# Performance work log

Hardware: AMD Instinct MI355X
Metric: run time of the kernel (lower is better)

## Reference

```python
import jax, jax.numpy as jnp
import numpy as np

N = 100000    # nodes
E = 1600000   # edges (avg degree 16)
IN = 128      # input feature dim
D = 32        # per-head hidden dim
H = 4         # heads for hidden layers
C = 16        # num_classes (final per-head dim)
NEG = 0.2     # leaky_relu negative slope


def setup_inputs() -> dict:
    key = jax.random.key(0)
    ks = jax.random.split(key, 14)
    s = jnp.float32(0.05)
    f32 = jnp.float32
    inp = {
        "inputs": jax.random.normal(ks[0], (N, IN), f32),
        "src": jax.random.randint(ks[1], (E,), 0, N),
        "dst": jax.random.randint(ks[2], (E,), 0, N),
        # layer 0: IN -> (H, D), no residual
        "W0": jax.random.normal(ks[3], (IN, H * D), f32) * s,
        "al0": jax.random.normal(ks[4], (H, D), f32) * s,
        "ar0": jax.random.normal(ks[5], (H, D), f32) * s,
        # layer 1: H*D -> (H, D), identity residual (dims match)
        "W1": jax.random.normal(ks[6], (H * D, H * D), f32) * s,
        "al1": jax.random.normal(ks[7], (H, D), f32) * s,
        "ar1": jax.random.normal(ks[8], (H, D), f32) * s,
        # final layer: H*D -> (1, C), linear residual projection
        "W2": jax.random.normal(ks[9], (H * D, 1 * C), f32) * s,
        "al2": jax.random.normal(ks[10], (1, C), f32) * s,
        "ar2": jax.random.normal(ks[11], (1, C), f32) * s,
        "resW2": jax.random.normal(ks[12], (H * D, 1 * C), f32) * s,
    }
    return inp


def gat_conv(h, W, al, ar, src, dst, n_heads, out_dim, res=None, act=None):
    # h: (N, F_in) -> out: (N, n_heads, out_dim)
    feat = (h @ W).reshape(N, n_heads, out_dim)            # (N,H,D)
    el = jnp.sum(feat * al, axis=-1)                       # (N,H)
    er = jnp.sum(feat * ar, axis=-1)                       # (N,H)
    e = jax.nn.leaky_relu(el[src] + er[dst], NEG)          # (E,H)
    # softmax over incoming edges per destination node
    emax = jax.ops.segment_max(e, dst, num_segments=N)     # (N,H)
    ex = jnp.exp(e - emax[dst])                            # (E,H)
    den = jax.ops.segment_sum(ex, dst, num_segments=N)     # (N,H)
    alpha = ex / den[dst]                                  # (E,H)
    msg = feat[src] * alpha[:, :, None]                    # (E,H,D) -- dominant traffic
    out = jax.ops.segment_sum(msg, dst, num_segments=N)    # (N,H,D)
    if res is not None:
        out = out + res
    if act is not None:
        out = act(out)
    return out


def reference(inputs, src, dst, W0, al0, ar0, W1, al1, ar1, W2, al2, ar2, resW2):
    # hidden layer 0 (no residual), GATConv activation = elu, then flatten + relu
    h = gat_conv(inputs, W0, al0, ar0, src, dst, H, D, res=None, act=jax.nn.elu)
    h = jax.nn.relu(h.reshape(N, H * D))
    # hidden layer 1, identity residual (in == H*D)
    res1 = h.reshape(N, H, D)
    h = gat_conv(h, W1, al1, ar1, src, dst, H, D, res=res1, act=jax.nn.elu)
    h = jax.nn.relu(h.reshape(N, H * D))
    # output layer: 1 head, linear residual projection, no activation, mean over heads
    res2 = (h @ resW2).reshape(N, 1, C)
    out = gat_conv(h, W2, al2, ar2, src, dst, 1, C, res=res2, act=None)
    return out.mean(axis=1)                                # (N, C)
```

## Files before the change

### kernel.cpp

```cpp
#include <hip/hip_runtime.h>

#define N_NODES 100000
#define N_EDGES 1600000
#define IN_F    128
#define NEG_SLOPE 0.2f
#define NBUCK   512
#define BCAP    5120
#define PCHUNK  4096
#define PGRID   391
#define GEMMGRID 1563

typedef __attribute__((ext_vector_type(8))) short bf16x8;
typedef __attribute__((ext_vector_type(4))) float f32x4;

__device__ __forceinline__ float bf2f(unsigned short u) {
    return __uint_as_float(((unsigned int)u) << 16);
}

__device__ __forceinline__ unsigned short f2bf(float f) {
    unsigned int u = __float_as_uint(f);
    u += 0x7FFFu + ((u >> 16) & 1u);
    return (unsigned short)(u >> 16);
}

__device__ __forceinline__ unsigned int ld_u32(const char* base, unsigned int off) {
    return *(const unsigned int*)(base + off);
}

__global__ __launch_bounds__(256) void init_pack(int* __restrict__ bcursor,
                                                 const float* __restrict__ W0,
                                                 const float* __restrict__ W1,
                                                 const float* __restrict__ W2,
                                                 const float* __restrict__ rW2,
                                                 unsigned short* __restrict__ W0p,
                                                 unsigned short* __restrict__ W1p,
                                                 unsigned short* __restrict__ W2p) {
    const int t = threadIdx.x;
    if (blockIdx.x < 2) {
        int i = blockIdx.x * 256 + t;
        if (i < NBUCK) bcursor[i] = i * BCAP;
        return;
    }
    int gid = (blockIdx.x - 2) * 256 + t;
    const float* W;
    unsigned short* Wp;
    int idx, ncols;
    if (gid < 16384)      { W = W0; Wp = W0p; idx = gid;          ncols = 128; }
    else if (gid < 32768) { W = W1; Wp = W1p; idx = gid - 16384;  ncols = 128; }
    else                  { W = W2; Wp = W2p; idx = gid - 32768;  ncols = 32;  }
    int j  = idx & 7;
    int l  = (idx >> 3) & 63;
    int kt = (idx >> 9) & 3;
    int nt = idx >> 11;
    int k  = kt * 32 + (l >> 4) * 8 + j;
    int n  = nt * 16 + (l & 15);
    float v;
    if (ncols == 128) v = W[k * 128 + n];
    else              v = (n < 16) ? W[k * 16 + n] : rW2[k * 16 + (n - 16)];
    Wp[idx] = f2bf(v);
}

__global__ __launch_bounds__(256) void part_gemm0(const int* __restrict__ src,
                                                  const int* __restrict__ dst,
                                                  int* __restrict__ bcursor,
                                                  unsigned int* __restrict__ pe, int nE,
                                                  const float* __restrict__ A,
                                                  const unsigned short* __restrict__ Wp,
                                                  const float* __restrict__ al,
                                                  const float* __restrict__ ar,
                                                  unsigned short* __restrict__ featb,
                                                  float* __restrict__ el,
                                                  float* __restrict__ er,
                                                  int nrows) {
    __shared__ int hist[NBUCK];
    __shared__ int lstart[NBUCK];
    __shared__ int gbase[NBUCK];
    __shared__ int curB[NBUCK];
    __shared__ int s[NBUCK];
    __shared__ unsigned int reorder[PCHUNK];

    const int t = threadIdx.x;

    if (blockIdx.x < PGRID) {
        const int start = blockIdx.x * PCHUNK;

        hist[t] = 0; hist[t + 256] = 0;
        __syncthreads();
#pragma unroll
        for (int j = 0; j < PCHUNK / 256; ++j) {
            int e = start + j * 256 + t;
            if (e < nE) atomicAdd(&hist[dst[e] >> 8], 1);
        }
        __syncthreads();
        const int c0 = hist[t];
        const int c1 = hist[t + 256];
        s[t] = c0; s[t + 256] = c1;
        __syncthreads();
#pragma unroll
        for (int off = 1; off <= 256; off <<= 1) {
            int x0 = (t >= off) ? s[t - off] : 0;
            int x1 = s[t + 256 - off];
            __syncthreads();
            s[t] += x0; s[t + 256] += x1;
            __syncthreads();
        }
        lstart[t]       = s[t] - c0;
        lstart[t + 256] = s[t + 256] - c1;
        curB[t]         = s[t] - c0;
        curB[t + 256]   = s[t + 256] - c1;
        gbase[t]        = c0 ? atomicAdd(&bcursor[t],       c0) : 0;
        gbase[t + 256]  = c1 ? atomicAdd(&bcursor[t + 256], c1) : 0;
        __syncthreads();

#pragma unroll
        for (int j = 0; j < PCHUNK / 256; ++j) {
            int e = start + j * 256 + t;
            if (e < nE) {
                int d  = dst[e];
                int sv = src[e];
                int b  = d >> 8;
                int pos = atomicAdd(&curB[b], 1);
                reorder[pos] = ((unsigned)sv << 8) | ((unsigned)d & 255u);
            }
        }
        __syncthreads();

        for (int b = t; b < NBUCK; b += 256) {
            int st = lstart[b];
            int en = curB[b];
            int gb = gbase[b];
            for (int k = st; k < en; ++k)
                pe[gb + (k - st)] = reorder[k];
        }
    } else {
        const int bid  = blockIdx.x - PGRID;
        const int wv   = t >> 6;
        const int lane = t & 63;
        const int q    = lane >> 4;
        const int m    = lane & 15;
        const int rb   = bid * 64 + wv * 16;
        const int arow = rb + m;
        const bool rok = arow < nrows;
        const float* Ar = A + (size_t)arow * IN_F;

        f32x4 acc[8];
#pragma unroll
        for (int nt = 0; nt < 8; ++nt) acc[nt] = (f32x4){0.f, 0.f, 0.f, 0.f};

#pragma unroll
        for (int kt = 0; kt < 4; ++kt) {
            bf16x8 afr = (bf16x8){0, 0, 0, 0, 0, 0, 0, 0};
            if (rok) {
                float4 v0 = *(const float4*)(Ar + kt * 32 + q * 8);
                float4 v1 = *(const float4*)(Ar + kt * 32 + q * 8 + 4);
                afr[0] = (short)f2bf(v0.x); afr[1] = (short)f2bf(v0.y);
                afr[2] = (short)f2bf(v0.z); afr[3] = (short)f2bf(v0.w);
                afr[4] = (short)f2bf(v1.x); afr[5] = (short)f2bf(v1.y);
                afr[6] = (short)f2bf(v1.z); afr[7] = (short)f2bf(v1.w);
            }
#pragma unroll
            for (int nt = 0; nt < 8; ++nt) {
                bf16x8 bfr = *(const bf16x8*)(Wp + ((size_t)(nt * 4 + kt) * 64 + lane) * 8);
                acc[nt] = __builtin_amdgcn_mfma_f32_16x16x32_bf16(afr, bfr, acc[nt], 0, 0, 0);
            }
        }

        float pel[16], per[16];
#pragma unroll
        for (int i = 0; i < 16; ++i) { pel[i] = 0.f; per[i] = 0.f; }

#pragma unroll
        for (int nt = 0; nt < 8; ++nt) {
            const int col = nt * 16 + m;
            const float alv = al[col];
            const float arv = ar[col];
            const int h = nt >> 1;
#pragma unroll
            for (int reg = 0; reg < 4; ++reg) {
                int row = rb + q * 4 + reg;
                float a = acc[nt][reg];
                if (row < nrows) featb[(size_t)row * 128 + col] = f2bf(a);
                pel[reg * 4 + h] += a * alv;
                per[reg * 4 + h] += a * arv;
            }
        }
#pragma unroll
        for (int sh = 8; sh > 0; sh >>= 1) {
#pragma unroll
            for (int i = 0; i < 16; ++i) {
                pel[i] += __shfl_down(pel[i], sh);
                per[i] += __shfl_down(per[i], sh);
            }
        }
        if (m == 0) {
#pragma unroll
            for (int reg = 0; reg < 4; ++reg) {
                int row = rb + q * 4 + reg;
                if (row < nrows) {
#pragma unroll
                    for (int h = 0; h < 4; ++h) {
                        el[row * 4 + h] = pel[reg * 4 + h];
                        er[row * 4 + h] = per[reg * 4 + h];
                    }
                }
            }
        }
    }
}

__global__ __launch_bounds__(256) void bucket_finalize(const unsigned int* __restrict__ pe,
                                                       const int* __restrict__ bcursor,
                                                       int* __restrict__ rowptr,
                                                       int* __restrict__ deg,
                                                       int* __restrict__ sorted_boff) {
    __shared__ int deg_l[256];
    __shared__ int s[256];
    __shared__ int cur[256];

    const int b  = blockIdx.x;
    const int t  = threadIdx.x;
    const int base = b * BCAP;
    const int cnt  = bcursor[b] - base;
    const int n    = b * 256 + t;

    deg_l[t] = 0;
    __syncthreads();
    for (int i = t; i < cnt; i += 256)
        atomicAdd(&deg_l[pe[base + i] & 255u], 1);
    __syncthreads();

    const int dv = deg_l[t];
    s[t] = dv;
    __syncthreads();
#pragma unroll
    for (int off = 1; off < 256; off <<= 1) {
        int x = (t >= off) ? s[t - off] : 0;
        __syncthreads();
        s[t] += x;
        __syncthreads();
    }
    const int off_l = s[t] - dv;
    if (n < N_NODES) {
        rowptr[n] = base + off_l;
        deg[n]    = dv;
    }
    cur[t] = off_l;
    __syncthreads();

    for (int i = t; i < cnt; i += 256) {
        unsigned int ed = pe[base + i];
        int pos = atomicAdd(&cur[ed & 255u], 1);
        sorted_boff[base + pos] = (int)(ed & 0xFFFFFF00u);
    }
}

__global__ __launch_bounds__(256) void gemm128_mfma_bf16(const unsigned short* __restrict__ Ab,
                                                         const unsigned short* __restrict__ Wp,
                                                         const float* __restrict__ al,
                                                         const float* __restrict__ ar,
                                                         unsigned short* __restrict__ featb,
                                                         float* __restrict__ el,
                                                         float* __restrict__ er,
                                                         int nrows) {
    const int t    = threadIdx.x;
    const int wv   = t >> 6;
    const int lane = t & 63;
    const int q    = lane >> 4;
    const int m    = lane & 15;
    const int rb   = blockIdx.x * 64 + wv * 16;
    const int arow = rb + m;
    const bool rok = arow < nrows;
    const unsigned short* Ar = Ab + (size_t)arow * IN_F;

    f32x4 acc[8];
#pragma unroll
    for (int nt = 0; nt < 8; ++nt) acc[nt] = (f32x4){0.f, 0.f, 0.f, 0.f};

#pragma unroll
    for (int kt = 0; kt < 4; ++kt) {
        bf16x8 afr = (bf16x8){0, 0, 0, 0, 0, 0, 0, 0};
        if (rok) afr = *(const bf16x8*)(Ar + kt * 32 + q * 8);
#pragma unroll
        for (int nt = 0; nt < 8; ++nt) {
            bf16x8 bfr = *(const bf16x8*)(Wp + ((size_t)(nt * 4 + kt) * 64 + lane) * 8);
            acc[nt] = __builtin_amdgcn_mfma_f32_16x16x32_bf16(afr, bfr, acc[nt], 0, 0, 0);
        }
    }

    float pel[16], per[16];
#pragma unroll
    for (int i = 0; i < 16; ++i) { pel[i] = 0.f; per[i] = 0.f; }

#pragma unroll
    for (int nt = 0; nt < 8; ++nt) {
        const int col = nt * 16 + m;
        const float alv = al[col];
        const float arv = ar[col];
        const int h = nt >> 1;
#pragma unroll
        for (int reg = 0; reg < 4; ++reg) {
            int row = rb + q * 4 + reg;
            float a = acc[nt][reg];
            if (row < nrows) featb[(size_t)row * 128 + col] = f2bf(a);
            pel[reg * 4 + h] += a * alv;
            per[reg * 4 + h] += a * arv;
        }
    }
#pragma unroll
    for (int sh = 8; sh > 0; sh >>= 1) {
#pragma unroll
        for (int i = 0; i < 16; ++i) {
            pel[i] += __shfl_down(pel[i], sh);
            per[i] += __shfl_down(per[i], sh);
        }
    }
    if (m == 0) {
#pragma unroll
        for (int reg = 0; reg < 4; ++reg) {
            int row = rb + q * 4 + reg;
            if (row < nrows) {
#pragma unroll
                for (int h = 0; h < 4; ++h) {
                    el[row * 4 + h] = pel[reg * 4 + h];
                    er[row * 4 + h] = per[reg * 4 + h];
                }
            }
        }
    }
}

__global__ __launch_bounds__(256) void gemm16_mfma(const unsigned short* __restrict__ Ab,
                                                   const unsigned short* __restrict__ Wp,
                                                   const float* __restrict__ al,
                                                   const float* __restrict__ ar,
                                                   unsigned short* __restrict__ feat2b,
                                                   float* __restrict__ res2,
                                                   float* __restrict__ el,
                                                   float* __restrict__ er,
                                                   int nrows) {
    const int t    = threadIdx.x;
    const int wv   = t >> 6;
    const int lane = t & 63;
    const int q    = lane >> 4;
    const int m    = lane & 15;
    const int rb   = blockIdx.x * 64 + wv * 16;
    const int arow = rb + m;
    const bool rok = arow < nrows;
    const unsigned short* Ar = Ab + (size_t)arow * IN_F;

    f32x4 acc0 = (f32x4){0.f, 0.f, 0.f, 0.f};
    f32x4 acc1 = (f32x4){0.f, 0.f, 0.f, 0.f};

#pragma unroll
    for (int kt = 0; kt < 4; ++kt) {
        bf16x8 afr = (bf16x8){0, 0, 0, 0, 0, 0, 0, 0};
        if (rok) afr = *(const bf16x8*)(Ar + kt * 32 + q * 8);
        bf16x8 b0 = *(const bf16x8*)(Wp + ((size_t)(0 * 4 + kt) * 64 + lane) * 8);
        bf16x8 b1 = *(const bf16x8*)(Wp + ((size_t)(1 * 4 + kt) * 64 + lane) * 8);
        acc0 = __builtin_amdgcn_mfma_f32_16x16x32_bf16(afr, b0, acc0, 0, 0, 0);
        acc1 = __builtin_amdgcn_mfma_f32_16x16x32_bf16(afr, b1, acc1, 0, 0, 0);
    }

    float pel[4], per[4];
    const float alv = al[m];
    const float arv = ar[m];
#pragma unroll
    for (int reg = 0; reg < 4; ++reg) {
        int row = rb + q * 4 + reg;
        float a = acc0[reg];
        if (row < nrows) {
            feat2b[(size_t)row * 16 + m] = f2bf(a);
            res2[(size_t)row * 16 + m]   = acc1[reg];
        }
        pel[reg] = a * alv;
        per[reg] = a * arv;
    }
#pragma unroll
    for (int sh = 8; sh > 0; sh >>= 1) {
#pragma unroll
        for (int reg = 0; reg < 4; ++reg) {
            pel[reg] += __shfl_down(pel[reg], sh);
            per[reg] += __shfl_down(per[reg], sh);
        }
    }
    if (m == 0) {
#pragma unroll
        for (int reg = 0; reg < 4; ++reg) {
            int row = rb + q * 4 + reg;
            if (row < nrows) { el[row] = pel[reg]; er[row] = per[reg]; }
        }
    }
}

__global__ __launch_bounds__(256) void gat_agg128(const int* __restrict__ rowptr,
                                                  const int* __restrict__ deg,
                                                  const int* __restrict__ sorted_boff,
                                                  const float* __restrict__ el,
                                                  const float* __restrict__ er,
                                                  const unsigned short* __restrict__ featb,
                                                  const unsigned short* __restrict__ resb,
                                                  unsigned short* __restrict__ outb) {
    __shared__ __align__(16) int   sS[4][64];
    __shared__ __align__(16) float sW[4][4][68];

    const int wv   = threadIdx.x >> 6;
    const int lane = threadIdx.x & 63;
    const int nd   = blockIdx.x * 4 + wv;

    const int dg = deg[nd];
    const int r0 = rowptr[nd];
    const int h  = lane >> 4;
    const unsigned int lane4 = (unsigned int)(lane << 2);
    const float4 er4 = *(const float4*)(er + nd * 4);
    const char* fb = (const char*)featb;
    const char* eb = (const char*)el;

    float dx = 0.f, dy = 0.f, dz = 0.f, dw = 0.f;
    float ax = 0.f, ay = 0.f;

    for (int base = 0; base < dg; base += 64) {
        int m = dg - base; if (m > 64) m = 64;

        int boff = 0;
        float4 w4 = {0.f, 0.f, 0.f, 0.f};
        if (lane < m) {
            boff = sorted_boff[r0 + base + lane];
            float4 e4 = *(const float4*)(eb + (unsigned int)(boff >> 4));
            float t_;
            t_ = e4.x + er4.x; t_ = t_ > 0.f ? t_ : NEG_SLOPE * t_; w4.x = __expf(t_);
            t_ = e4.y + er4.y; t_ = t_ > 0.f ? t_ : NEG_SLOPE * t_; w4.y = __expf(t_);
            t_ = e4.z + er4.z; t_ = t_ > 0.f ? t_ : NEG_SLOPE * t_; w4.z = __expf(t_);
            t_ = e4.w + er4.w; t_ = t_ > 0.f ? t_ : NEG_SLOPE * t_; w4.w = __expf(t_);
        }
        sS[wv][lane]    = boff;
        sW[wv][0][lane] = w4.x;
        sW[wv][1][lane] = w4.y;
        sW[wv][2][lane] = w4.z;
        sW[wv][3][lane] = w4.w;
        dx += w4.x; dy += w4.y; dz += w4.z; dw += w4.w;

        const int mr = (m + 7) & ~7;
        for (int i = 0; i < mr; i += 8) {
            const int4   sa = *(const int4*)(&sS[wv][i]);
            const int4   sb = *(const int4*)(&sS[wv][i + 4]);
            const float4 wa = *(const float4*)(&sW[wv][h][i]);
            const float4 wb = *(const float4*)(&sW[wv][h][i + 4]);

            unsigned int u0 = ld_u32(fb, (unsigned int)sa.x + lane4);
            unsigned int u1 = ld_u32(fb, (unsigned int)sa.y + lane4);
            unsigned int u2 = ld_u32(fb, (unsigned int)sa.z + lane4);
            unsigned int u3 = ld_u32(fb, (unsigned int)sa.w + lane4);
            unsigned int u4 = ld_u32(fb, (unsigned int)sb.x + lane4);
            unsigned int u5 = ld_u32(fb, (unsigned int)sb.y + lane4);
            unsigned int u6 = ld_u32(fb, (unsigned int)sb.z + lane4);
            unsigned int u7 = ld_u32(fb, (unsigned int)sb.w + lane4);

            ax += wa.x * __uint_as_float(u0 << 16);
            ay += wa.x * __uint_as_float(u0 & 0xFFFF0000u);
            ax += wa.y * __uint_as_float(u1 << 16);
            ay += wa.y * __uint_as_float(u1 & 0xFFFF0000u);
            ax += wa.z * __uint_as_float(u2 << 16);
            ay += wa.z * __uint_as_float(u2 & 0xFFFF0000u);
            ax += wa.w * __uint_as_float(u3 << 16);
            ay += wa.w * __uint_as_float(u3 & 0xFFFF0000u);
            ax += wb.x * __uint_as_float(u4 << 16);
            ay += wb.x * __uint_as_float(u4 & 0xFFFF0000u);
            ax += wb.y * __uint_as_float(u5 << 16);
            ay += wb.y * __uint_as_float(u5 & 0xFFFF0000u);
            ax += wb.z * __uint_as_float(u6 << 16);
            ay += wb.z * __uint_as_float(u6 & 0xFFFF0000u);
            ax += wb.w * __uint_as_float(u7 << 16);
            ay += wb.w * __uint_as_float(u7 & 0xFFFF0000u);
        }
    }

#pragma unroll
    for (int sh = 1; sh < 64; sh <<= 1) {
        dx += __shfl_xor(dx, sh);
        dy += __shfl_xor(dy, sh);
        dz += __shfl_xor(dz, sh);
        dw += __shfl_xor(dw, sh);
    }
    float den = (h == 0) ? dx : (h == 1) ? dy : (h == 2) ? dz : dw;

    float scale = den > 0.f ? 1.f / den : 0.f;
    float ox = ax * scale, oy = ay * scale;
    size_t o0 = (size_t)nd * 128 + lane * 2;
    if (resb) {
        ushort2 rv = *(const ushort2*)(resb + o0);
        ox += bf2f(rv.x);
        oy += bf2f(rv.y);
    }
    ox = fmaxf(ox, 0.f);
    oy = fmaxf(oy, 0.f);
    ushort2 ou;
    ou.x = f2bf(ox);
    ou.y = f2bf(oy);
    *(ushort2*)(outb + o0) = ou;
}

__global__ __launch_bounds__(256) void gat_agg16(const int* __restrict__ rowptr,
                                                 const int* __restrict__ deg,
                                                 const int* __restrict__ sorted_boff,
                                                 const float* __restrict__ el,
                                                 const float* __restrict__ er,
                                                 const unsigned short* __restrict__ feat2b,
                                                 const float* __restrict__ res,
                                                 float* __restrict__ out) {
    __shared__ int   sS[4][64];
    __shared__ float sW[4][64];

    const int wv   = threadIdx.x >> 6;
    const int lane = threadIdx.x & 63;
    const int nd   = blockIdx.x * 4 + (threadIdx.x >> 6);
    const int g    = lane >> 3;
    const unsigned int flane4 = (unsigned int)((lane & 7) << 2);
    const char* f2base = (const char*)feat2b;
    const char* eb = (const char*)el;

    const int dg = deg[nd];
    const int r0 = rowptr[nd];
    const float erd = er[nd];

    float ax = 0.f, ay = 0.f, den = 0.f;

    for (int base = 0; base < dg; base += 64) {
        int m = dg - base; if (m > 64) m = 64;
        if (lane < m) {
            int boff = sorted_boff[r0 + base + lane];
            sS[wv][lane] = boff;
            float v = *(const float*)(eb + (unsigned int)(boff >> 6)) + erd;
            v = v > 0.f ? v : NEG_SLOPE * v;
            sW[wv][lane] = __expf(v);
        }
        for (int i = g; i < m; i += 8) {
            int bo  = sS[wv][i];
            float w = sW[wv][i];
            den += w;
            unsigned int u = *(const unsigned int*)(f2base + (unsigned int)(bo >> 3) + flane4);
            ax += w * __uint_as_float(u << 16);
            ay += w * __uint_as_float(u & 0xFFFF0000u);
        }
    }

    ax += __shfl_down(ax, 32); ay += __shfl_down(ay, 32); den += __shfl_down(den, 32);
    ax += __shfl_down(ax, 16); ay += __shfl_down(ay, 16); den += __shfl_down(den, 16);
    ax += __shfl_down(ax, 8);  ay += __shfl_down(ay, 8);  den += __shfl_down(den, 8);

    if (lane < 8) {
        float scale = den > 0.f ? 1.f / den : 0.f;
        size_t o0 = (size_t)nd * 16 + ((lane & 7) << 1);
        float2 o;
        o.x = ax * scale + res[o0];
        o.y = ay * scale + res[o0 + 1];
        *(float2*)(out + o0) = o;
    }
}

extern "C" void kernel_launch(void* const* d_in, const int* in_sizes, int n_in,
                              void* d_out, int out_size, void* d_ws, size_t ws_size,
                              hipStream_t stream) {
    const float* inputs = (const float*)d_in[0];
    const int*   src    = (const int*)d_in[1];
    const int*   dst    = (const int*)d_in[2];
    const float* W0     = (const float*)d_in[3];
    const float* al0    = (const float*)d_in[4];
    const float* ar0    = (const float*)d_in[5];
    const float* W1     = (const float*)d_in[6];
    const float* al1    = (const float*)d_in[7];
    const float* ar1    = (const float*)d_in[8];
    const float* W2     = (const float*)d_in[9];
    const float* al2    = (const float*)d_in[10];
    const float* ar2    = (const float*)d_in[11];
    const float* resW2  = (const float*)d_in[12];
    float* out = (float*)d_out;

    const size_t NF = (size_t)N_NODES * 128;
    float* ws   = (float*)d_ws;
    float* el   = ws;
    float* er   = el + (size_t)N_NODES * 4;
    float* res2 = er + (size_t)N_NODES * 4;
    unsigned short* hbufb  = (unsigned short*)(res2 + (size_t)N_NODES * 16);
    unsigned short* featb  = hbufb + NF;
    unsigned short* feat2b = featb + NF;
    unsigned short* W0p    = feat2b + (size_t)N_NODES * 16;
    unsigned short* W1p    = W0p + 16384;
    unsigned short* W2p    = W1p + 16384;
    int* iws = (int*)(W2p + 8192);
    unsigned int* pe = (unsigned int*)iws;
    int* sorted_boff = iws + NBUCK * BCAP;
    int* deg         = sorted_boff + NBUCK * BCAP;
    int* rowptr      = deg + N_NODES;
    int* bcursor     = rowptr + N_NODES;

    dim3 blk(256);
    int aggGrid = N_NODES / 4;

    init_pack<<<162, blk, 0, stream>>>(bcursor, W0, W1, W2, resW2, W0p, W1p, W2p);
    part_gemm0<<<PGRID + GEMMGRID, blk, 0, stream>>>(src, dst, bcursor, pe, N_EDGES,
                                                     inputs, W0p, al0, ar0, featb,
                                                     el, er, N_NODES);
    bucket_finalize<<<PGRID, blk, 0, stream>>>(pe, bcursor, rowptr, deg, sorted_boff);

    gat_agg128<<<aggGrid, blk, 0, stream>>>(rowptr, deg, sorted_boff, el, er, featb,
                                            nullptr, hbufb);

    gemm128_mfma_bf16<<<GEMMGRID, blk, 0, stream>>>(hbufb, W1p, al1, ar1, featb,
                                                    el, er, N_NODES);
    gat_agg128<<<aggGrid, blk, 0, stream>>>(rowptr, deg, sorted_boff, el, er, featb,
                                            hbufb, hbufb);

    gemm16_mfma<<<GEMMGRID, blk, 0, stream>>>(hbufb, W2p, al2, ar2, feat2b, res2,
                                              el, er, N_NODES);
    gat_agg16<<<aggGrid, blk, 0, stream>>>(rowptr, deg, sorted_boff, el, er, feat2b,
                                           res2, out);
}
```

Baseline: 377.4 us.

## Fold weight packing into partition kernel, stage weights in LDS, sort edges by source

Removes the separate init_pack launch. The zeroing of bucket counters becomes a memset, W0 is packed per block into LDS inside the fused GEMM, and W1/W2 packing runs in extra blocks of the same launch. gemm128 now stages its packed weights in shared memory instead of reading them from global memory. bucket_finalize sub-bins edges by their high source bits so each node's edge list is roughly sorted by source, which should improve gather locality in the aggregation kernels. In exchange, every GEMM block repacks W0 redundantly and uses more LDS, which may lower occupancy.

```diff
diff --git a/kernel.cpp b/kernel.cpp
--- a/kernel.cpp
+++ b/kernel.cpp
@@ -9,6 +9,8 @@
 #define PCHUNK  4096
 #define PGRID   391
 #define GEMMGRID 1563
+#define PACKGRID 96
+#define SBIN    25
 
 typedef __attribute__((ext_vector_type(8))) short bf16x8;
 typedef __attribute__((ext_vector_type(4))) float f32x4;
@@ -27,61 +29,35 @@
     return *(const unsigned int*)(base + off);
 }
 
-__global__ __launch_bounds__(256) void init_pack(int* __restrict__ bcursor,
-                                                 const float* __restrict__ W0,
-                                                 const float* __restrict__ W1,
-                                                 const float* __restrict__ W2,
-                                                 const float* __restrict__ rW2,
-                                                 unsigned short* __restrict__ W0p,
-                                                 unsigned short* __restrict__ W1p,
-                                                 unsigned short* __restrict__ W2p) {
-    const int t = threadIdx.x;
-    if (blockIdx.x < 2) {
-        int i = blockIdx.x * 256 + t;
-        if (i < NBUCK) bcursor[i] = i * BCAP;
-        return;
-    }
-    int gid = (blockIdx.x - 2) * 256 + t;
-    const float* W;
-    unsigned short* Wp;
-    int idx, ncols;
-    if (gid < 16384)      { W = W0; Wp = W0p; idx = gid;          ncols = 128; }
-    else if (gid < 32768) { W = W1; Wp = W1p; idx = gid - 16384;  ncols = 128; }
-    else                  { W = W2; Wp = W2p; idx = gid - 32768;  ncols = 32;  }
-    int j  = idx & 7;
-    int l  = (idx >> 3) & 63;
-    int kt = (idx >> 9) & 3;
-    int nt = idx >> 11;
-    int k  = kt * 32 + (l >> 4) * 8 + j;
-    int n  = nt * 16 + (l & 15);
-    float v;
-    if (ncols == 128) v = W[k * 128 + n];
-    else              v = (n < 16) ? W[k * 16 + n] : rW2[k * 16 + (n - 16)];
-    Wp[idx] = f2bf(v);
-}
-
 __global__ __launch_bounds__(256) void part_gemm0(const int* __restrict__ src,
                                                   const int* __restrict__ dst,
-                                                  int* __restrict__ bcursor,
+                                                  int* __restrict__ bcount,
                                                   unsigned int* __restrict__ pe, int nE,
                                                   const float* __restrict__ A,
-                                                  const unsigned short* __restrict__ Wp,
+                                                  const float* __restrict__ W0,
                                                   const float* __restrict__ al,
                                                   const float* __restrict__ ar,
                                                   unsigned short* __restrict__ featb,
                                                   float* __restrict__ el,
                                                   float* __restrict__ er,
-                                                  int nrows) {
-    __shared__ int hist[NBUCK];
-    __shared__ int lstart[NBUCK];
-    __shared__ int gbase[NBUCK];
-    __shared__ int curB[NBUCK];
-    __shared__ int s[NBUCK];
-    __shared__ unsigned int reorder[PCHUNK];
+                                                  int nrows,
+                                                  const float* __restrict__ W1,
+                                                  const float* __restrict__ W2,
+                                                  const float* __restrict__ rW2,
+                                                  unsigned short* __restrict__ W1p,
+                                                  unsigned short* __restrict__ W2p) {
+    __shared__ int shbuf[8192];
 
     const int t = threadIdx.x;
 
     if (blockIdx.x < PGRID) {
+        int* hist   = shbuf;
+        int* lstart = shbuf + 512;
+        int* gbase  = shbuf + 1024;
+        int* curB   = shbuf + 1536;
+        int* s      = shbuf + 2048;
+        unsigned int* reorder = (unsigned int*)(shbuf + 2560);
+
         const int start = blockIdx.x * PCHUNK;
 
         hist[t] = 0; hist[t + 256] = 0;
@@ -108,8 +84,8 @@
         lstart[t + 256] = s[t + 256] - c1;
         curB[t]         = s[t] - c0;
         curB[t + 256]   = s[t + 256] - c1;
-        gbase[t]        = c0 ? atomicAdd(&bcursor[t],       c0) : 0;
-        gbase[t + 256]  = c1 ? atomicAdd(&bcursor[t + 256], c1) : 0;
+        gbase[t]        = c0 ? t * BCAP + atomicAdd(&bcount[t], c0) : 0;
+        gbase[t + 256]  = c1 ? (t + 256) * BCAP + atomicAdd(&bcount[t + 256], c1) : 0;
         __syncthreads();
 
 #pragma unroll
@@ -132,7 +108,23 @@
             for (int k = st; k < en; ++k)
                 pe[gb + (k - st)] = reorder[k];
         }
-    } else {
+    } else if (blockIdx.x < PGRID + GEMMGRID) {
+        unsigned short* wl = (unsigned short*)shbuf;
+#pragma unroll
+        for (int w = 0; w < 16; ++w) {
+            int e = (w * 256 + t) * 4;
+            float4 v = *(const float4*)(W0 + e);
+            int r = e >> 7, c = e & 127;
+            int kt = r >> 5, j = r & 7, lhi = (r >> 3) & 3;
+            int nt = c >> 4;
+            int ib = ((nt * 4 + kt) * 64 + lhi * 16 + (c & 15)) * 8 + j;
+            wl[ib]      = f2bf(v.x);
+            wl[ib + 8]  = f2bf(v.y);
+            wl[ib + 16] = f2bf(v.z);
+            wl[ib + 24] = f2bf(v.w);
+        }
+        __syncthreads();
+
         const int bid  = blockIdx.x - PGRID;
         const int wv   = t >> 6;
         const int lane = t & 63;
@@ -160,7 +152,7 @@
             }
 #pragma unroll
             for (int nt = 0; nt < 8; ++nt) {
-                bf16x8 bfr = *(const bf16x8*)(Wp + ((size_t)(nt * 4 + kt) * 64 + lane) * 8);
+                bf16x8 bfr = *(const bf16x8*)(wl + ((nt * 4 + kt) * 64 + lane) * 8);
                 acc[nt] = __builtin_amdgcn_mfma_f32_16x16x32_bf16(afr, bfr, acc[nt], 0, 0, 0);
             }
         }
@@ -205,31 +197,53 @@
                 }
             }
         }
+    } else {
+        int gid = (int)(blockIdx.x - (PGRID + GEMMGRID)) * 256 + t;
+        const float* W;
+        unsigned short* Wp2;
+        int idx, ncols;
+        if (gid < 16384) { W = W1; Wp2 = W1p; idx = gid;          ncols = 128; }
+        else             { W = W2; Wp2 = W2p; idx = gid - 16384;  ncols = 32;  }
+        int j  = idx & 7;
+        int l  = (idx >> 3) & 63;
+        int kt = (idx >> 9) & 3;
+        int nt = idx >> 11;
+        int k  = kt * 32 + (l >> 4) * 8 + j;
+        int nn = nt * 16 + (l & 15);
+        float v;
+        if (ncols == 128) v = W[k * 128 + nn];
+        else              v = (nn < 16) ? W[k * 16 + nn] : rW2[k * 16 + (nn - 16)];
+        Wp2[idx] = f2bf(v);
     }
 }
 
 __global__ __launch_bounds__(256) void bucket_finalize(const unsigned int* __restrict__ pe,
-                                                       const int* __restrict__ bcursor,
+                                                       const int* __restrict__ bcount,
                                                        int* __restrict__ rowptr,
                                                        int* __restrict__ deg,
                                                        int* __restrict__ sorted_boff) {
-    __shared__ int deg_l[256];
+    __shared__ int binh[256 * SBIN];
     __shared__ int s[256];
-    __shared__ int cur[256];
 
     const int b  = blockIdx.x;
     const int t  = threadIdx.x;
     const int base = b * BCAP;
-    const int cnt  = bcursor[b] - base;
+    const int cnt  = bcount[b];
     const int n    = b * 256 + t;
 
-    deg_l[t] = 0;
+#pragma unroll
+    for (int k = 0; k < SBIN; ++k) binh[t * SBIN + k] = 0;
     __syncthreads();
-    for (int i = t; i < cnt; i += 256)
-        atomicAdd(&deg_l[pe[base + i] & 255u], 1);
+
+    for (int i = t; i < cnt; i += 256) {
+        unsigned int e = pe[base + i];
+        atomicAdd(&binh[(e & 255u) * SBIN + (e >> 20)], 1);
+    }
     __syncthreads();
 
-    const int dv = deg_l[t];
+    int dv = 0;
+#pragma unroll
+    for (int k = 0; k < SBIN; ++k) dv += binh[t * SBIN + k];
     s[t] = dv;
     __syncthreads();
 #pragma unroll
@@ -244,13 +258,19 @@
         rowptr[n] = base + off_l;
         deg[n]    = dv;
     }
-    cur[t] = off_l;
+    int run = off_l;
+#pragma unroll
+    for (int k = 0; k < SBIN; ++k) {
+        int v = binh[t * SBIN + k];
+        binh[t * SBIN + k] = run;
+        run += v;
+    }
     __syncthreads();
 
     for (int i = t; i < cnt; i += 256) {
-        unsigned int ed = pe[base + i];
-        int pos = atomicAdd(&cur[ed & 255u], 1);
-        sorted_boff[base + pos] = (int)(ed & 0xFFFFFF00u);
+        unsigned int e = pe[base + i];
+        int pos = atomicAdd(&binh[(e & 255u) * SBIN + (e >> 20)], 1);
+        sorted_boff[base + pos] = (int)(e & 0xFFFFFF00u);
     }
 }
 
@@ -262,7 +282,13 @@
                                                          float* __restrict__ el,
                                                          float* __restrict__ er,
                                                          int nrows) {
+    __shared__ int4 wl4[2048];
     const int t    = threadIdx.x;
+#pragma unroll
+    for (int w = 0; w < 8; ++w) wl4[w * 256 + t] = ((const int4*)Wp)[w * 256 + t];
+    __syncthreads();
+    const unsigned short* wl = (const unsigned short*)wl4;
+
     const int wv   = t >> 6;
     const int lane = t & 63;
     const int q    = lane >> 4;
@@ -282,7 +308,7 @@
         if (rok) afr = *(const bf16x8*)(Ar + kt * 32 + q * 8);
 #pragma unroll
         for (int nt = 0; nt < 8; ++nt) {
-            bf16x8 bfr = *(const bf16x8*)(Wp + ((size_t)(nt * 4 + kt) * 64 + lane) * 8);
+            bf16x8 bfr = *(const bf16x8*)(wl + ((size_t)(nt * 4 + kt) * 64 + lane) * 8);
             acc[nt] = __builtin_amdgcn_mfma_f32_16x16x32_bf16(afr, bfr, acc[nt], 0, 0, 0);
         }
     }
@@ -583,24 +609,25 @@
     unsigned short* hbufb  = (unsigned short*)(res2 + (size_t)N_NODES * 16);
     unsigned short* featb  = hbufb + NF;
     unsigned short* feat2b = featb + NF;
-    unsigned short* W0p    = feat2b + (size_t)N_NODES * 16;
-    unsigned short* W1p    = W0p + 16384;
+    unsigned short* W1p    = feat2b + (size_t)N_NODES * 16;
     unsigned short* W2p    = W1p + 16384;
     int* iws = (int*)(W2p + 8192);
     unsigned int* pe = (unsigned int*)iws;
     int* sorted_boff = iws + NBUCK * BCAP;
     int* deg         = sorted_boff + NBUCK * BCAP;
     int* rowptr      = deg + N_NODES;
-    int* bcursor     = rowptr + N_NODES;
+    int* bcount      = rowptr + N_NODES;
 
     dim3 blk(256);
     int aggGrid = N_NODES / 4;
 
-    init_pack<<<162, blk, 0, stream>>>(bcursor, W0, W1, W2, resW2, W0p, W1p, W2p);
-    part_gemm0<<<PGRID + GEMMGRID, blk, 0, stream>>>(src, dst, bcursor, pe, N_EDGES,
-                                                     inputs, W0p, al0, ar0, featb,
-                                                     el, er, N_NODES);
-    bucket_finalize<<<PGRID, blk, 0, stream>>>(pe, bcursor, rowptr, deg, sorted_boff);
+    hipMemsetAsync(bcount, 0, NBUCK * sizeof(int), stream);
+
+    part_gemm0<<<PGRID + GEMMGRID + PACKGRID, blk, 0, stream>>>(
+        src, dst, bcount, pe, N_EDGES, inputs, W0, al0, ar0, featb, el, er,
+        N_NODES, W1, W2, resW2, W1p, W2p);
+
+    bucket_finalize<<<PGRID, blk, 0, stream>>>(pe, bcount, rowptr, deg, sorted_boff);
 
     gat_agg128<<<aggGrid, blk, 0, stream>>>(rowptr, deg, sorted_boff, el, er, featb,
                                             nullptr, hbufb);
```

Measured after the change: 386.7 us. 2.5% more time.

## Gather 8-byte feature chunks with half-wave edge split and stage GEMM weights in LDS

Applied to the files above, without the earlier changes.

The 128-wide aggregation kernel now has each half-wave own a different parity of edges. Each lane loads 8 bytes (4 bf16) per edge instead of 4 bytes, which halves the gather instructions per edge, and the two halves are combined with one cross-half shuffle at the end. Separately, the MFMA GEMM first copies the packed 32KB weight matrix into shared memory and reads the B fragments from there instead of global memory. The cost is an extra reduction step, idle lanes during the epilogue, and 32KB of LDS per GEMM block, which could lower occupancy.

```diff
diff --git a/kernel.cpp b/kernel.cpp
--- a/kernel.cpp
+++ b/kernel.cpp
@@ -25,6 +25,9 @@
 
 __device__ __forceinline__ unsigned int ld_u32(const char* base, unsigned int off) {
     return *(const unsigned int*)(base + off);
+}
+__device__ __forceinline__ uint2 ld_u64(const char* base, unsigned int off) {
+    return *(const uint2*)(base + off);
 }
 
 __global__ __launch_bounds__(256) void init_pack(int* __restrict__ bcursor,
@@ -262,7 +265,13 @@
                                                          float* __restrict__ el,
                                                          float* __restrict__ er,
                                                          int nrows) {
+    __shared__ int4 wl4[2048];
     const int t    = threadIdx.x;
+#pragma unroll
+    for (int w = 0; w < 8; ++w) wl4[w * 256 + t] = ((const int4*)Wp)[w * 256 + t];
+    __syncthreads();
+    const unsigned short* wl = (const unsigned short*)wl4;
+
     const int wv   = t >> 6;
     const int lane = t & 63;
     const int q    = lane >> 4;
@@ -282,7 +291,7 @@
         if (rok) afr = *(const bf16x8*)(Ar + kt * 32 + q * 8);
 #pragma unroll
         for (int nt = 0; nt < 8; ++nt) {
-            bf16x8 bfr = *(const bf16x8*)(Wp + ((size_t)(nt * 4 + kt) * 64 + lane) * 8);
+            bf16x8 bfr = *(const bf16x8*)(wl + ((size_t)(nt * 4 + kt) * 64 + lane) * 8);
             acc[nt] = __builtin_amdgcn_mfma_f32_16x16x32_bf16(afr, bfr, acc[nt], 0, 0, 0);
         }
     }
@@ -400,23 +409,25 @@
                                                   const unsigned short* __restrict__ featb,
                                                   const unsigned short* __restrict__ resb,
                                                   unsigned short* __restrict__ outb) {
-    __shared__ __align__(16) int   sS[4][64];
-    __shared__ __align__(16) float sW[4][4][68];
+    __shared__ __align__(16) int   sSp[4][2][32];
+    __shared__ __align__(16) float sW2[4][4][2][36];
 
     const int wv   = threadIdx.x >> 6;
     const int lane = threadIdx.x & 63;
+    const int half = lane >> 5;
+    const int sub  = lane & 31;
+    const int h    = sub >> 3;
+    const unsigned int lane8 = (unsigned int)(sub << 3);
     const int nd   = blockIdx.x * 4 + wv;
 
     const int dg = deg[nd];
     const int r0 = rowptr[nd];
-    const int h  = lane >> 4;
-    const unsigned int lane4 = (unsigned int)(lane << 2);
     const float4 er4 = *(const float4*)(er + nd * 4);
     const char* fb = (const char*)featb;
     const char* eb = (const char*)el;
 
     float dx = 0.f, dy = 0.f, dz = 0.f, dw = 0.f;
-    float ax = 0.f, ay = 0.f;
+    float a0 = 0.f, a1 = 0.f, a2 = 0.f, a3 = 0.f;
 
     for (int base = 0; base < dg; base += 64) {
         int m = dg - base; if (m > 64) m = 64;
@@ -432,47 +443,46 @@
             t_ = e4.z + er4.z; t_ = t_ > 0.f ? t_ : NEG_SLOPE * t_; w4.z = __expf(t_);
             t_ = e4.w + er4.w; t_ = t_ > 0.f ? t_ : NEG_SLOPE * t_; w4.w = __expf(t_);
         }
-        sS[wv][lane]    = boff;
-        sW[wv][0][lane] = w4.x;
-        sW[wv][1][lane] = w4.y;
-        sW[wv][2][lane] = w4.z;
-        sW[wv][3][lane] = w4.w;
+        sSp[wv][lane & 1][lane >> 1]    = boff;
+        sW2[wv][0][lane & 1][lane >> 1] = w4.x;
+        sW2[wv][1][lane & 1][lane >> 1] = w4.y;
+        sW2[wv][2][lane & 1][lane >> 1] = w4.z;
+        sW2[wv][3][lane & 1][lane >> 1] = w4.w;
         dx += w4.x; dy += w4.y; dz += w4.z; dw += w4.w;
 
-        const int mr = (m + 7) & ~7;
-        for (int i = 0; i < mr; i += 8) {
-            const int4   sa = *(const int4*)(&sS[wv][i]);
-            const int4   sb = *(const int4*)(&sS[wv][i + 4]);
-            const float4 wa = *(const float4*)(&sW[wv][h][i]);
-            const float4 wb = *(const float4*)(&sW[wv][h][i + 4]);
-
-            unsigned int u0 = ld_u32(fb, (unsigned int)sa.x + lane4);
-            unsigned int u1 = ld_u32(fb, (unsigned int)sa.y + lane4);
-            unsigned int u2 = ld_u32(fb, (unsigned int)sa.z + lane4);
-            unsigned int u3 = ld_u32(fb, (unsigned int)sa.w + lane4);
-            unsigned int u4 = ld_u32(fb, (unsigned int)sb.x + lane4);
-            unsigned int u5 = ld_u32(fb, (unsigned int)sb.y + lane4);
-            unsigned int u6 = ld_u32(fb, (unsigned int)sb.z + lane4);
-            unsigned int u7 = ld_u32(fb, (unsigned int)sb.w + lane4);
-
-            ax += wa.x * __uint_as_float(u0 << 16);
-            ay += wa.x * __uint_as_float(u0 & 0xFFFF0000u);
-            ax += wa.y * __uint_as_float(u1 << 16);
-            ay += wa.y * __uint_as_float(u1 & 0xFFFF0000u);
-            ax += wa.z * __uint_as_float(u2 << 16);
-            ay += wa.z * __uint_as_float(u2 & 0xFFFF0000u);
-            ax += wa.w * __uint_as_float(u3 << 16);
-            ay += wa.w * __uint_as_float(u3 & 0xFFFF0000u);
-            ax += wb.x * __uint_as_float(u4 << 16);
-            ay += wb.x * __uint_as_float(u4 & 0xFFFF0000u);
-            ax += wb.y * __uint_as_float(u5 << 16);
-            ay += wb.y * __uint_as_float(u5 & 0xFFFF0000u);
-            ax += wb.z * __uint_as_float(u6 << 16);
-            ay += wb.z * __uint_as_float(u6 & 0xFFFF0000u);
-            ax += wb.w * __uint_as_float(u7 << 16);
-            ay += wb.w * __uint_as_float(u7 & 0xFFFF0000u);
-        }
-    }
+        const int pr = ((m + 7) & ~7) >> 1;
+        for (int p = 0; p < pr; p += 4) {
+            const int4   sa = *(const int4*)(&sSp[wv][half][p]);
+            const float4 wa = *(const float4*)(&sW2[wv][h][half][p]);
+
+            uint2 u0 = ld_u64(fb, (unsigned int)sa.x + lane8);
+            uint2 u1 = ld_u64(fb, (unsigned int)sa.y + lane8);
+            uint2 u2 = ld_u64(fb, (unsigned int)sa.z + lane8);
+            uint2 u3 = ld_u64(fb, (unsigned int)sa.w + lane8);
+
+            a0 += wa.x * __uint_as_float(u0.x << 16);
+            a1 += wa.x * __uint_as_float(u0.x & 0xFFFF0000u);
+            a2 += wa.x * __uint_as_float(u0.y << 16);
+            a3 += wa.x * __uint_as_float(u0.y & 0xFFFF0000u);
+            a0 += wa.y * __uint_as_float(u1.x << 16);
+            a1 += wa.y * __uint_as_float(u1.x & 0xFFFF0000u);
+            a2 += wa.y * __uint_as_float(u1.y << 16);
+            a3 += wa.y * __uint_as_float(u1.y & 0xFFFF0000u);
+            a0 += wa.z * __uint_as_float(u2.x << 16);
+            a1 += wa.z * __uint_as_float(u2.x & 0xFFFF0000u);
+            a2 += wa.z * __uint_as_float(u2.y << 16);
+            a3 += wa.z * __uint_as_float(u2.y & 0xFFFF0000u);
+            a0 += wa.w * __uint_as_float(u3.x << 16);
+            a1 += wa.w * __uint_as_float(u3.x & 0xFFFF0000u);
+            a2 += wa.w * __uint_as_float(u3.y << 16);
+            a3 += wa.w * __uint_as_float(u3.y & 0xFFFF0000u);
+        }
+    }
+
+    a0 += __shfl_xor(a0, 32);
+    a1 += __shfl_xor(a1, 32);
+    a2 += __shfl_xor(a2, 32);
+    a3 += __shfl_xor(a3, 32);
 
 #pragma unroll
     for (int sh = 1; sh < 64; sh <<= 1) {
@@ -483,20 +493,26 @@
     }
     float den = (h == 0) ? dx : (h == 1) ? dy : (h == 2) ? dz : dw;
 
-    float scale = den > 0.f ? 1.f / den : 0.f;
-    float ox = ax * scale, oy = ay * scale;
-    size_t o0 = (size_t)nd * 128 + lane * 2;
-    if (resb) {
-        ushort2 rv = *(const ushort2*)(resb + o0);
-        ox += bf2f(rv.x);
-        oy += bf2f(rv.y);
-    }
-    ox = fmaxf(ox, 0.f);
-    oy = fmaxf(oy, 0.f);
-    ushort2 ou;
-    ou.x = f2bf(ox);
-    ou.y = f2bf(oy);
-    *(ushort2*)(outb + o0) = ou;
+    if (lane < 32) {
+        float scale = den > 0.f ? 1.f / den : 0.f;
+        float o0 = a0 * scale, o1 = a1 * scale, o2 = a2 * scale, o3 = a3 * scale;
+        size_t ob = (size_t)nd * 128 + sub * 4;
+        if (resb) {
+            uint2 rv = *(const uint2*)(resb + ob);
+            o0 += __uint_as_float(rv.x << 16);
+            o1 += __uint_as_float(rv.x & 0xFFFF0000u);
+            o2 += __uint_as_float(rv.y << 16);
+            o3 += __uint_as_float(rv.y & 0xFFFF0000u);
+        }
+        o0 = fmaxf(o0, 0.f);
+        o1 = fmaxf(o1, 0.f);
+        o2 = fmaxf(o2, 0.f);
+        o3 = fmaxf(o3, 0.f);
+        uint2 ou;
+        ou.x = (unsigned int)f2bf(o0) | ((unsigned int)f2bf(o1) << 16);
+        ou.y = (unsigned int)f2bf(o2) | ((unsigned int)f2bf(o3) << 16);
+        *(uint2*)(outb + ob) = ou;
+    }
 }
 
 __global__ __launch_bounds__(256) void gat_agg16(const int* __restrict__ rowptr,
```

Result: slower. 385.3 us (+2.1%).

## Fold attention vectors into weights and compute el/er via extra MFMA; widen agg16 loads

Applied to the files above, without the earlier changes.

Precomputes W·al and W·ar per head as an extra bf16 B-matrix tile, so each GEMM gets el/er from one additional MFMA. This replaces the per-column FMA accumulation and the 16-register shuffle reduction in the epilogue. It also reworks gat_agg16 so each lane loads 8 bytes (4 bf16 features) and 16 edges are processed concurrently per wave, with xor-shuffle reduction and float4 output. The trade-off is that el/er now come from the bf16-rounded folded weights instead of fp32 sums of the features, which may shift attention logits slightly.

```diff
diff --git a/kernel.cpp b/kernel.cpp
--- a/kernel.cpp
+++ b/kernel.cpp
@@ -26,6 +26,9 @@
 __device__ __forceinline__ unsigned int ld_u32(const char* base, unsigned int off) {
     return *(const unsigned int*)(base + off);
 }
+__device__ __forceinline__ uint2 ld_u64(const char* base, unsigned int off) {
+    return *(const uint2*)(base + off);
+}
 
 __global__ __launch_bounds__(256) void init_pack(int* __restrict__ bcursor,
                                                  const float* __restrict__ W0,
@@ -34,30 +37,75 @@
                                                  const float* __restrict__ rW2,
                                                  unsigned short* __restrict__ W0p,
                                                  unsigned short* __restrict__ W1p,
-                                                 unsigned short* __restrict__ W2p) {
+                                                 unsigned short* __restrict__ W2p,
+                                                 const float* __restrict__ al0,
+                                                 const float* __restrict__ ar0,
+                                                 const float* __restrict__ al1,
+                                                 const float* __restrict__ ar1,
+                                                 const float* __restrict__ al2,
+                                                 const float* __restrict__ ar2,
+                                                 unsigned short* __restrict__ Walp0,
+                                                 unsigned short* __restrict__ Walp1,
+                                                 unsigned short* __restrict__ Walp2) {
     const int t = threadIdx.x;
     if (blockIdx.x < 2) {
         int i = blockIdx.x * 256 + t;
         if (i < NBUCK) bcursor[i] = i * BCAP;
         return;
     }
-    int gid = (blockIdx.x - 2) * 256 + t;
-    const float* W;
-    unsigned short* Wp;
-    int idx, ncols;
-    if (gid < 16384)      { W = W0; Wp = W0p; idx = gid;          ncols = 128; }
-    else if (gid < 32768) { W = W1; Wp = W1p; idx = gid - 16384;  ncols = 128; }
-    else                  { W = W2; Wp = W2p; idx = gid - 32768;  ncols = 32;  }
-    int j  = idx & 7;
-    int l  = (idx >> 3) & 63;
-    int kt = (idx >> 9) & 3;
-    int nt = idx >> 11;
-    int k  = kt * 32 + (l >> 4) * 8 + j;
-    int n  = nt * 16 + (l & 15);
-    float v;
-    if (ncols == 128) v = W[k * 128 + n];
-    else              v = (n < 16) ? W[k * 16 + n] : rW2[k * 16 + (n - 16)];
-    Wp[idx] = f2bf(v);
+    if (blockIdx.x < 162) {
+        int gid = (blockIdx.x - 2) * 256 + t;
+        const float* W;
+        unsigned short* Wp;
+        int idx, ncols;
+        if (gid < 16384)      { W = W0; Wp = W0p; idx = gid;          ncols = 128; }
+        else if (gid < 32768) { W = W1; Wp = W1p; idx = gid - 16384;  ncols = 128; }
+        else                  { W = W2; Wp = W2p; idx = gid - 32768;  ncols = 32;  }
+        int j  = idx & 7;
+        int l  = (idx >> 3) & 63;
+        int kt = (idx >> 9) & 3;
+        int nt = idx >> 11;
+        int k  = kt * 32 + (l >> 4) * 8 + j;
+        int n  = nt * 16 + (l & 15);
+        float v;
+        if (ncols == 128) v = W[k * 128 + n];
+        else              v = (n < 16) ? W[k * 16 + n] : rW2[k * 16 + (n - 16)];
+        Wp[idx] = f2bf(v);
+        return;
+    }
+    if (blockIdx.x < 164) {
+        const float* W  = (blockIdx.x == 162) ? W0 : W1;
+        const float* al = (blockIdx.x == 162) ? al0 : al1;
+        const float* ar = (blockIdx.x == 162) ? ar0 : ar1;
+        unsigned short* Wa = (blockIdx.x == 162) ? Walp0 : Walp1;
+        for (int e = t; e < 2048; e += 256) {
+            int k = e >> 4, c = e & 15;
+            float s = 0.f;
+            if (c < 8) {
+                int h = c & 3;
+                const float* av = (c < 4) ? al : ar;
+                const float* wr = W + k * 128 + h * 32;
+#pragma unroll
+                for (int d = 0; d < 32; ++d) s += wr[d] * av[h * 32 + d];
+            }
+            int kt = k >> 5, rem = k & 31;
+            int lane = (rem >> 3) * 16 + c, j = rem & 7;
+            Wa[(kt * 64 + lane) * 8 + j] = f2bf(s);
+        }
+        return;
+    }
+    for (int e = t; e < 2048; e += 256) {
+        int k = e >> 4, c = e & 15;
+        float s = 0.f;
+        if (c < 2) {
+            const float* av = (c == 0) ? al2 : ar2;
+#pragma unroll
+            for (int cc = 0; cc < 16; ++cc) s += W2[k * 16 + cc] * av[cc];
+        }
+        int kt = k >> 5, rem = k & 31;
+        int lane = (rem >> 3) * 16 + c, j = rem & 7;
+        Walp2[(kt * 64 + lane) * 8 + j] = f2bf(s);
+    }
 }
 
 __global__ __launch_bounds__(256) void part_gemm0(const int* __restrict__ src,
@@ -66,8 +114,7 @@
                                                   unsigned int* __restrict__ pe, int nE,
                                                   const float* __restrict__ A,
                                                   const unsigned short* __restrict__ Wp,
-                                                  const float* __restrict__ al,
-                                                  const float* __restrict__ ar,
+                                                  const unsigned short* __restrict__ Walp,
                                                   unsigned short* __restrict__ featb,
                                                   float* __restrict__ el,
                                                   float* __restrict__ er,
@@ -146,6 +193,7 @@
         f32x4 acc[8];
 #pragma unroll
         for (int nt = 0; nt < 8; ++nt) acc[nt] = (f32x4){0.f, 0.f, 0.f, 0.f};
+        f32x4 acc_a = (f32x4){0.f, 0.f, 0.f, 0.f};
 
 #pragma unroll
         for (int kt = 0; kt < 4; ++kt) {
@@ -163,46 +211,26 @@
                 bf16x8 bfr = *(const bf16x8*)(Wp + ((size_t)(nt * 4 + kt) * 64 + lane) * 8);
                 acc[nt] = __builtin_amdgcn_mfma_f32_16x16x32_bf16(afr, bfr, acc[nt], 0, 0, 0);
             }
-        }
-
-        float pel[16], per[16];
-#pragma unroll
-        for (int i = 0; i < 16; ++i) { pel[i] = 0.f; per[i] = 0.f; }
+            bf16x8 wfr = *(const bf16x8*)(Walp + ((size_t)kt * 64 + lane) * 8);
+            acc_a = __builtin_amdgcn_mfma_f32_16x16x32_bf16(afr, wfr, acc_a, 0, 0, 0);
+        }
 
 #pragma unroll
         for (int nt = 0; nt < 8; ++nt) {
             const int col = nt * 16 + m;
-            const float alv = al[col];
-            const float arv = ar[col];
-            const int h = nt >> 1;
 #pragma unroll
             for (int reg = 0; reg < 4; ++reg) {
                 int row = rb + q * 4 + reg;
-                float a = acc[nt][reg];
-                if (row < nrows) featb[(size_t)row * 128 + col] = f2bf(a);
-                pel[reg * 4 + h] += a * alv;
-                per[reg * 4 + h] += a * arv;
+                if (row < nrows) featb[(size_t)row * 128 + col] = f2bf(acc[nt][reg]);
             }
         }
-#pragma unroll
-        for (int sh = 8; sh > 0; sh >>= 1) {
-#pragma unroll
-            for (int i = 0; i < 16; ++i) {
-                pel[i] += __shfl_down(pel[i], sh);
-                per[i] += __shfl_down(per[i], sh);
-            }
-        }
-        if (m == 0) {
+        if (m < 8) {
+            float* dstp = (m < 4) ? el : er;
+            const int hh = m & 3;
 #pragma unroll
             for (int reg = 0; reg < 4; ++reg) {
                 int row = rb + q * 4 + reg;
-                if (row < nrows) {
-#pragma unroll
-                    for (int h = 0; h < 4; ++h) {
-                        el[row * 4 + h] = pel[reg * 4 + h];
-                        er[row * 4 + h] = per[reg * 4 + h];
-                    }
-                }
+                if (row < nrows) dstp[row * 4 + hh] = acc_a[reg];
             }
         }
     }
@@ -256,8 +284,7 @@
 
 __global__ __launch_bounds__(256) void gemm128_mfma_bf16(const unsigned short* __restrict__ Ab,
                                                          const unsigned short* __restrict__ Wp,
-                                                         const float* __restrict__ al,
-                                                         const float* __restrict__ ar,
+                                                         const unsigned short* __restrict__ Walp,
                                                          unsigned short* __restrict__ featb,
                                                          float* __restrict__ el,
                                                          float* __restrict__ er,
@@ -275,6 +302,7 @@
     f32x4 acc[8];
 #pragma unroll
     for (int nt = 0; nt < 8; ++nt) acc[nt] = (f32x4){0.f, 0.f, 0.f, 0.f};
+    f32x4 acc_a = (f32x4){0.f, 0.f, 0.f, 0.f};
 
 #pragma unroll
     for (int kt = 0; kt < 4; ++kt) {
@@ -285,54 +313,33 @@
             bf16x8 bfr = *(const bf16x8*)(Wp + ((size_t)(nt * 4 + kt) * 64 + lane) * 8);
             acc[nt] = __builtin_amdgcn_mfma_f32_16x16x32_bf16(afr, bfr, acc[nt], 0, 0, 0);
         }
-    }
-
-    float pel[16], per[16];
-#pragma unroll
-    for (int i = 0; i < 16; ++i) { pel[i] = 0.f; per[i] = 0.f; }
+        bf16x8 wfr = *(const bf16x8*)(Walp + ((size_t)kt * 64 + lane) * 8);
+        acc_a = __builtin_amdgcn_mfma_f32_16x16x32_bf16(afr, wfr, acc_a, 0, 0, 0);
+    }
 
 #pragma unroll
     for (int nt = 0; nt < 8; ++nt) {
         const int col = nt * 16 + m;
-        const float alv = al[col];
-        const float arv = ar[col];
-        const int h = nt >> 1;
 #pragma unroll
         for (int reg = 0; reg < 4; ++reg) {
             int row = rb + q * 4 + reg;
-            float a = acc[nt][reg];
-            if (row < nrows) featb[(size_t)row * 128 + col] = f2bf(a);
-            pel[reg * 4 + h] += a * alv;
-            per[reg * 4 + h] += a * arv;
-        }
-    }
-#pragma unroll
-    for (int sh = 8; sh > 0; sh >>= 1) {
-#pragma unroll
-        for (int i = 0; i < 16; ++i) {
-            pel[i] += __shfl_down(pel[i], sh);
-            per[i] += __shfl_down(per[i], sh);
-        }
-    }
-    if (m == 0) {
+            if (row < nrows) featb[(size_t)row * 128 + col] = f2bf(acc[nt][reg]);
+        }
+    }
+    if (m < 8) {
+        float* dstp = (m < 4) ? el : er;
+        const int hh = m & 3;
 #pragma unroll
         for (int reg = 0; reg < 4; ++reg) {
             int row = rb + q * 4 + reg;
-            if (row < nrows) {
-#pragma unroll
-                for (int h = 0; h < 4; ++h) {
-                    el[row * 4 + h] = pel[reg * 4 + h];
-                    er[row * 4 + h] = per[reg * 4 + h];
-                }
-            }
+            if (row < nrows) dstp[row * 4 + hh] = acc_a[reg];
         }
     }
 }
 
 __global__ __launch_bounds__(256) void gemm16_mfma(const unsigned short* __restrict__ Ab,
                                                    const unsigned short* __restrict__ Wp,
-                                                   const float* __restrict__ al,
-                                                   const float* __restrict__ ar,
+                                                   const unsigned short* __restrict__ Walp,
                                                    unsigned short* __restrict__ feat2b,
                                                    float* __restrict__ res2,
                                                    float* __restrict__ el,
@@ -350,6 +357,7 @@
 
     f32x4 acc0 = (f32x4){0.f, 0.f, 0.f, 0.f};
     f32x4 acc1 = (f32x4){0.f, 0.f, 0.f, 0.f};
+    f32x4 acc_a = (f32x4){0.f, 0.f, 0.f, 0.f};
 
 #pragma unroll
     for (int kt = 0; kt < 4; ++kt) {
@@ -359,35 +367,24 @@
         bf16x8 b1 = *(const bf16x8*)(Wp + ((size_t)(1 * 4 + kt) * 64 + lane) * 8);
         acc0 = __builtin_amdgcn_mfma_f32_16x16x32_bf16(afr, b0, acc0, 0, 0, 0);
         acc1 = __builtin_amdgcn_mfma_f32_16x16x32_bf16(afr, b1, acc1, 0, 0, 0);
-    }
-
-    float pel[4], per[4];
-    const float alv = al[m];
-    const float arv = ar[m];
+        bf16x8 wfr = *(const bf16x8*)(Walp + ((size_t)kt * 64 + lane) * 8);
+        acc_a = __builtin_amdgcn_mfma_f32_16x16x32_bf16(afr, wfr, acc_a, 0, 0, 0);
+    }
+
 #pragma unroll
     for (int reg = 0; reg < 4; ++reg) {
         int row = rb + q * 4 + reg;
-        float a = acc0[reg];
         if (row < nrows) {
-            feat2b[(size_t)row * 16 + m] = f2bf(a);
+            feat2b[(size_t)row * 16 + m] = f2bf(acc0[reg]);
             res2[(size_t)row * 16 + m]   = acc1[reg];
         }
-        pel[reg] = a * alv;
-        per[reg] = a * arv;
-    }
-#pragma unroll
-    for (int sh = 8; sh > 0; sh >>= 1) {
-#pragma unroll
-        for (int reg = 0; reg < 4; ++reg) {
-            pel[reg] += __shfl_down(pel[reg], sh);
-            per[reg] += __shfl_down(per[reg], sh);
-        }
-    }
-    if (m == 0) {
+    }
+    if (m < 2) {
+        float* dstp = (m == 0) ? el : er;
 #pragma unroll
         for (int reg = 0; reg < 4; ++reg) {
             int row = rb + q * 4 + reg;
-            if (row < nrows) { el[row] = pel[reg]; er[row] = per[reg]; }
+            if (row < nrows) dstp[row] = acc_a[reg];
         }
     }
 }
@@ -512,9 +509,9 @@
 
     const int wv   = threadIdx.x >> 6;
     const int lane = threadIdx.x & 63;
-    const int nd   = blockIdx.x * 4 + (threadIdx.x >> 6);
-    const int g    = lane >> 3;
-    const unsigned int flane4 = (unsigned int)((lane & 7) << 2);
+    const int nd   = blockIdx.x * 4 + wv;
+    const int grp  = lane >> 2;
+    const unsigned int fo = (unsigned int)((lane & 3) << 3);
     const char* f2base = (const char*)feat2b;
     const char* eb = (const char*)el;
 
@@ -522,7 +519,7 @@
     const int r0 = rowptr[nd];
     const float erd = er[nd];
 
-    float ax = 0.f, ay = 0.f, den = 0.f;
+    float a0 = 0.f, a1 = 0.f, a2 = 0.f, a3 = 0.f, den = 0.f;
 
     for (int base = 0; base < dg; base += 64) {
         int m = dg - base; if (m > 64) m = 64;
@@ -533,27 +530,36 @@
             v = v > 0.f ? v : NEG_SLOPE * v;
             sW[wv][lane] = __expf(v);
         }
-        for (int i = g; i < m; i += 8) {
+        for (int i = grp; i < m; i += 16) {
             int bo  = sS[wv][i];
             float w = sW[wv][i];
             den += w;
-            unsigned int u = *(const unsigned int*)(f2base + (unsigned int)(bo >> 3) + flane4);
-            ax += w * __uint_as_float(u << 16);
-            ay += w * __uint_as_float(u & 0xFFFF0000u);
-        }
-    }
-
-    ax += __shfl_down(ax, 32); ay += __shfl_down(ay, 32); den += __shfl_down(den, 32);
-    ax += __shfl_down(ax, 16); ay += __shfl_down(ay, 16); den += __shfl_down(den, 16);
-    ax += __shfl_down(ax, 8);  ay += __shfl_down(ay, 8);  den += __shfl_down(den, 8);
-
-    if (lane < 8) {
+            uint2 u = ld_u64(f2base, (unsigned int)(bo >> 3) + fo);
+            a0 += w * __uint_as_float(u.x << 16);
+            a1 += w * __uint_as_float(u.x & 0xFFFF0000u);
+            a2 += w * __uint_as_float(u.y << 16);
+            a3 += w * __uint_as_float(u.y & 0xFFFF0000u);
+        }
+    }
+
+#pragma unroll
+    for (int sh = 4; sh < 64; sh <<= 1) {
+        a0 += __shfl_xor(a0, sh);
+        a1 += __shfl_xor(a1, sh);
+        a2 += __shfl_xor(a2, sh);
+        a3 += __shfl_xor(a3, sh);
+        den += __shfl_xor(den, sh);
+    }
+
+    if (lane < 4) {
         float scale = den > 0.f ? 1.f / den : 0.f;
-        size_t o0 = (size_t)nd * 16 + ((lane & 7) << 1);
-        float2 o;
-        o.x = ax * scale + res[o0];
-        o.y = ay * scale + res[o0 + 1];
-        *(float2*)(out + o0) = o;
+        size_t ob = (size_t)nd * 16 + lane * 4;
+        float4 o;
+        o.x = a0 * scale + res[ob];
+        o.y = a1 * scale + res[ob + 1];
+        o.z = a2 * scale + res[ob + 2];
+        o.w = a3 * scale + res[ob + 3];
+        *(float4*)(out + ob) = o;
     }
 }
 
@@ -586,7 +592,10 @@
     unsigned short* W0p    = feat2b + (size_t)N_NODES * 16;
     unsigned short* W1p    = W0p + 16384;
     unsigned short* W2p    = W1p + 16384;
-    int* iws = (int*)(W2p + 8192);
+    unsigned short* Walp0  = W2p + 8192;
+    unsigned short* Walp1  = Walp0 + 2048;
+    unsigned short* Walp2  = Walp1 + 2048;
+    int* iws = (int*)(Walp2 + 2048);
     unsigned int* pe = (unsigned int*)iws;
     int* sorted_boff = iws + NBUCK * BCAP;
     int* deg         = sorted_boff + NBUCK * BCAP;
@@ -596,21 +605,23 @@
     dim3 blk(256);
     int aggGrid = N_NODES / 4;
 
-    init_pack<<<162, blk, 0, stream>>>(bcursor, W0, W1, W2, resW2, W0p, W1p, W2p);
+    init_pack<<<165, blk, 0, stream>>>(bcursor, W0, W1, W2, resW2, W0p, W1p, W2p,
+                                       al0, ar0, al1, ar1, al2, ar2,
+                                       Walp0, Walp1, Walp2);
     part_gemm0<<<PGRID + GEMMGRID, blk, 0, stream>>>(src, dst, bcursor, pe, N_EDGES,
-                                                     inputs, W0p, al0, ar0, featb,
+                                                     inputs, W0p, Walp0, featb,
                                                      el, er, N_NODES);
     bucket_finalize<<<PGRID, blk, 0, stream>>>(pe, bcursor, rowptr, deg, sorted_boff);
 
     gat_agg128<<<aggGrid, blk, 0, stream>>>(rowptr, deg, sorted_boff, el, er, featb,
                                             nullptr, hbufb);
 
-    gemm128_mfma_bf16<<<GEMMGRID, blk, 0, stream>>>(hbufb, W1p, al1, ar1, featb,
+    gemm128_mfma_bf16<<<GEMMGRID, blk, 0, stream>>>(hbufb, W1p, Walp1, featb,
                                                     el, er, N_NODES);
     gat_agg128<<<aggGrid, blk, 0, stream>>>(rowptr, deg, sorted_boff, el, er, featb,
                                             hbufb, hbufb);
 
-    gemm16_mfma<<<GEMMGRID, blk, 0, stream>>>(hbufb, W2p, al2, ar2, feat2b, res2,
+    gemm16_mfma<<<GEMMGRID, blk, 0, stream>>>(hbufb, W2p, Walp2, feat2b, res2,
                                               el, er, N_NODES);
     gat_agg16<<<aggGrid, blk, 0, stream>>>(rowptr, deg, sorted_boff, el, er, feat2b,
                                            res2, out);
```

After: 383.6 us. About the same (+1.6%).
